# Optimization experiments

Measured on AMD Instinct MI355X. Metric: run time of the kernel, lower is better.

Reference implementation:

```python
import jax, jax.numpy as jnp
import numpy as np

SEQ, BATCH, IN, HS = 512, 64, 512, 1024
FORGET_BIAS = 0.0

def setup_inputs() -> dict:
    key = jax.random.key(0)
    ks = jax.random.split(key, 6)
    stdv = 1.0 / np.sqrt(HS)
    u = lambda k, shape: jax.random.uniform(k, shape, jnp.float32, -stdv, stdv)
    return {
        "x": jax.random.normal(ks[0], (SEQ, BATCH, IN), jnp.float32),
        "W": u(ks[1], (IN + HS, 4 * HS)),
        "bias": u(ks[2], (4 * HS,)),
        "peep_i": u(ks[3], (HS,)),
        "peep_f": u(ks[4], (HS,)),
        "peep_o": u(ks[5], (HS,)),
    }

def reference(x, W, bias, peep_i, peep_f, peep_o):
    bs = x.shape[1]
    c0 = jnp.zeros((bs, HS), x.dtype)
    h0 = jnp.zeros((bs, HS), x.dtype)

    def step(carry, x_t):
        c, h = carry
        # gates: [B, 4H] = [x_t | h] @ W + bias
        gates = jnp.concatenate([x_t, h], axis=1) @ W + bias
        i_t, j_t, f_t, o_t = jnp.split(gates, 4, axis=1)
        c_new = (jax.nn.sigmoid(f_t + FORGET_BIAS + c * peep_f) * c
                 + jax.nn.sigmoid(i_t + c * peep_i) * jnp.tanh(j_t))
        h_new = jax.nn.sigmoid(o_t + c_new * peep_o) * jnp.tanh(c_new)
        return (c_new, h_new), h_new

    (c_T, h_T), hidden_seq = jax.lax.scan(step, (c0, h0), x)
    return hidden_seq, (c_T, h_T)
```

## Files before the change

kernel.cpp:

```cpp
#include <hip/hip_runtime.h>
#include <hip/hip_bf16.h>


#define SEQN 512
#define BATCH 64
#define INDIM 512
#define HSZ 1024
#define NWG 128
#define DEPTH 64

typedef __attribute__((ext_vector_type(8))) short s16x8;
typedef __attribute__((ext_vector_type(4))) float f32x4;
typedef __attribute__((ext_vector_type(2))) float f32x2;
typedef __attribute__((ext_vector_type(4))) int i32x4;
typedef unsigned long long u64;

__device__ __forceinline__ short f2bf(float f) {
  __hip_bfloat16 b = __float2bfloat16(f);
  short s;
  __builtin_memcpy(&s, &b, 2);
  return s;
}
__device__ __forceinline__ float sigf(float x) { return 1.f / (1.f + __expf(-x)); }
__device__ __forceinline__ float tanh_fast(float x) { return 2.f / (1.f + __expf(-2.f * x)) - 1.f; }

__global__ __launch_bounds__(256) void prep_w(const float* __restrict__ W,
                                              short* __restrict__ WxP,
                                              short* __restrict__ WhP) {
  int idx = blockIdx.x * 256 + threadIdx.x;
  if (idx >= 1536 * 4096) return;
  int k = idx >> 12, col = idx & 4095;
  short b = f2bf(W[idx]);
  int gate = col >> 10, hidx = col & 1023;
  int g = hidx >> 3, off = hidx & 7;
  int pc = off * 4 + gate;
  if (k < 512) {
    WxP[(size_t)(((g * 64 + (k >> 3)) * 32 + pc) << 3) + (k & 7)] = b;
  } else {
    int kh = k - 512;
    WhP[(size_t)(((g * 128 + (kh >> 3)) * 32 + pc) << 3) + (kh & 7)] = b;
  }
}

__global__ __launch_bounds__(256) void prep_x(const float* __restrict__ x,
                                              short* __restrict__ xbp) {
  int idx = blockIdx.x * 256 + threadIdx.x;
  if (idx >= SEQN * 64 * 64) return;
  int kb = idx & 63, m = (idx >> 6) & 63, t = idx >> 12;
  const float4* xp = reinterpret_cast<const float4*>(x + ((size_t)t * 64 + m) * 512 + kb * 8);
  float4 a = xp[0], c = xp[1];
  s16x8 v;
  v[0] = f2bf(a.x); v[1] = f2bf(a.y); v[2] = f2bf(a.z); v[3] = f2bf(a.w);
  v[4] = f2bf(c.x); v[5] = f2bf(c.y); v[6] = f2bf(c.z); v[7] = f2bf(c.w);
  reinterpret_cast<s16x8*>(xbp)[((size_t)t * 64 + kb) * 64 + m] = v;
}

__global__ __launch_bounds__(256, 1) void lstm_seq(const short* __restrict__ xbp,
                                                   const short* __restrict__ WhP,
                                                   const short* __restrict__ WxP,
                                                   const float* __restrict__ bias,
                                                   const float* __restrict__ peep_i,
                                                   const float* __restrict__ peep_f,
                                                   const float* __restrict__ peep_o,
                                                   u64* hqt,
                                                   float* __restrict__ out) {
  __shared__ short WhS[32768];
  __shared__ short WxS[16384];
  __shared__ float outS[512];
  int g = blockIdx.x;
  int tid = threadIdx.x, w = tid >> 6, l = tid & 63;
  {
    const s16x8* src = reinterpret_cast<const s16x8*>(WhP + (size_t)g * 32768);
    s16x8* dst = reinterpret_cast<s16x8*>(WhS);
#pragma unroll
    for (int i = 0; i < 16; ++i) dst[i * 256 + tid] = src[i * 256 + tid];
    const s16x8* src2 = reinterpret_cast<const s16x8*>(WxP + (size_t)g * 16384);
    s16x8* dst2 = reinterpret_cast<s16x8*>(WxS);
#pragma unroll
    for (int i = 0; i < 8; ++i) dst2[i * 256 + tid] = src2[i * 256 + tid];
  }
  int m = w * 16 + (l & 15), q4 = l >> 4, l15 = l & 15;
  int c0 = g * 8 + q4, c1 = c0 + 4;
  float bi0 = bias[c0], bj0 = bias[1024 + c0], bf0 = bias[2048 + c0], bo0 = bias[3072 + c0];
  float bi1 = bias[c1], bj1 = bias[1024 + c1], bf1 = bias[2048 + c1], bo1 = bias[3072 + c1];
  float pi0 = peep_i[c0], pf0 = peep_f[c0], po0 = peep_o[c0];
  float pi1 = peep_i[c1], pf1 = peep_f[c1], po1 = peep_o[c1];
  float cr0 = 0.f, cr1 = 0.f;
  s16x8* WhS16 = reinterpret_cast<s16x8*>(WhS);
  s16x8* WxS16 = reinterpret_cast<s16x8*>(WxS);
  __syncthreads();

#define LOADG(BANK, G)                                                                   \
  {                                                                                      \
    _Pragma("unroll") for (int i = 0; i < 16; ++i) {                                     \
      int kb_ = ((G) * 8 + (i >> 1)) * 4 + q4;                                           \
      BANK[i] = *reinterpret_cast<const i32x4*>(rdq + kb_ * 256 + m * 4 + (i & 1) * 2);  \
    }                                                                                    \
  }
#define RELOADG(BANK, G)                                                                 \
  {                                                                                      \
    _Pragma("unroll") for (int i = 0; i < 16; ++i) {                                     \
      int kb_ = ((G) * 8 + (i >> 1)) * 4 + q4;                                           \
      const u64* p_ = rdq + kb_ * 256 + m * 4 + (i & 1) * 2;                             \
      asm volatile("global_load_dwordx4 %0, %1, off sc0 sc1" : "=v"(BANK[i]) : "v"(p_)); \
    }                                                                                    \
    asm volatile("s_waitcnt vmcnt(0)" ::: "memory");                                     \
    __builtin_amdgcn_sched_barrier(0);                                                   \
  }
#define CHECKG(BANK, G)                                                                  \
  {                                                                                      \
    int guard = 0;                                                                       \
    while (true) {                                                                       \
      bool ok = true;                                                                    \
      _Pragma("unroll") for (int i = 0; i < 16; ++i) ok &=                               \
          ((unsigned)BANK[i][1] == (unsigned)t) & ((unsigned)BANK[i][3] == (unsigned)t); \
      if (__all((int)ok)) break;                                                         \
      if (++guard > (1 << 13)) break;                         \
      RELOADG(BANK, G);                                                                  \
    }                                                                                    \
  }
#define MFMAG(BANK, G)                                                                   \
  {                                                                                      \
    _Pragma("unroll") for (int kk2 = 0; kk2 < 8; ++kk2) {                                \
      int kb_ = ((G) * 8 + kk2) * 4 + q4;                                                \
      unsigned d0 = (unsigned)BANK[kk2 * 2][0], d1 = (unsigned)BANK[kk2 * 2][2];         \
      unsigned d2 = (unsigned)BANK[kk2 * 2 + 1][0], d3 = (unsigned)BANK[kk2 * 2 + 1][2]; \
      union { unsigned u[4]; s16x8 v; } bu;                                              \
      bu.u[0] = (d0 & 0xFFFFu) | (d1 << 16);                                             \
      bu.u[1] = (d2 & 0xFFFFu) | (d3 << 16);                                             \
      bu.u[2] = (d0 >> 16) | (d1 & 0xFFFF0000u);                                         \
      bu.u[3] = (d2 >> 16) | (d3 & 0xFFFF0000u);                                        \
      s16x8 a0 = WhS16[kb_ * 32 + l15];                                                  \
      s16x8 a1 = WhS16[kb_ * 32 + 16 + l15];                                             \
      acc0 = __builtin_amdgcn_mfma_f32_16x16x32_bf16(a0, bu.v, acc0, 0, 0, 0);           \
      acc1 = __builtin_amdgcn_mfma_f32_16x16x32_bf16(a1, bu.v, acc1, 0, 0, 0);           \
    }                                                                                    \
  }

  for (int t = 0; t < SEQN; ++t) {
    f32x4 acc0 = {0.f, 0.f, 0.f, 0.f}, acc1 = {0.f, 0.f, 0.f, 0.f};
    {
      const s16x8* xt = reinterpret_cast<const s16x8*>(xbp) + (size_t)t * 4096;
#pragma unroll 4
      for (int kk = 0; kk < 16; ++kk) {
        int kb = kk * 4 + q4;
        s16x8 bx = xt[kb * 64 + m];
        s16x8 a0 = WxS16[kb * 32 + l15];
        s16x8 a1 = WxS16[kb * 32 + 16 + l15];
        acc0 = __builtin_amdgcn_mfma_f32_16x16x32_bf16(a0, bx, acc0, 0, 0, 0);
        acc1 = __builtin_amdgcn_mfma_f32_16x16x32_bf16(a1, bx, acc1, 0, 0, 0);
      }
    }
    if (t > 0) {
      const u64* rdq = hqt + (size_t)(t & (DEPTH - 1)) * 32768;
      i32x4 hA[16], hB[16];
      LOADG(hA, 0);
      LOADG(hB, 1);
      CHECKG(hA, 0);
      MFMAG(hA, 0);
      LOADG(hA, 2);
      CHECKG(hB, 1);
      MFMAG(hB, 1);
      LOADG(hB, 3);
      CHECKG(hA, 2);
      MFMAG(hA, 2);
      CHECKG(hB, 3);
      MFMAG(hB, 3);
    }
    float i0 = sigf(acc0[0] + bi0 + cr0 * pi0);
    float f0 = sigf(acc0[2] + bf0 + cr0 * pf0);
    float cn0 = f0 * cr0 + i0 * tanh_fast(acc0[1] + bj0);
    float o0 = sigf(acc0[3] + bo0 + cn0 * po0);
    float h0 = o0 * tanh_fast(cn0);
    cr0 = cn0;
    float i1 = sigf(acc1[0] + bi1 + cr1 * pi1);
    float f1 = sigf(acc1[2] + bf1 + cr1 * pf1);
    float cn1 = f1 * cr1 + i1 * tanh_fast(acc1[1] + bj1);
    float o1 = sigf(acc1[3] + bo1 + cn1 * po1);
    float h1 = o1 * tanh_fast(cn1);
    cr1 = cn1;
    {
      u64 q = ((u64)(unsigned)(t + 1) << 32) |
              ((u64)(unsigned short)f2bf(h1) << 16) | (u64)(unsigned short)f2bf(h0);
      (void)__hip_atomic_exchange(
          hqt + (size_t)((t + 1) & (DEPTH - 1)) * 32768 + g * 256 + m * 4 + q4, q,
          __ATOMIC_RELAXED, __HIP_MEMORY_SCOPE_AGENT);
    }
    outS[w * 128 + l15 * 8 + q4] = h0;
    outS[w * 128 + l15 * 8 + q4 + 4] = h1;
    {
      f32x2 v = *reinterpret_cast<f32x2*>(&outS[w * 128 + (l >> 2) * 8 + (l & 3) * 2]);
      int row = w * 16 + (l >> 2), col = g * 8 + (l & 3) * 2;
      __builtin_nontemporal_store(
          v, reinterpret_cast<f32x2*>(out + (size_t)t * 65536 + (size_t)row * 1024 + col));
    }
    if (t == SEQN - 1) {
      out[33554432ull + (size_t)m * 1024 + c0] = cn0;
      out[33554432ull + (size_t)m * 1024 + c1] = cn1;
      out[33619968ull + (size_t)m * 1024 + c0] = h0;
      out[33619968ull + (size_t)m * 1024 + c1] = h1;
    }
  }
#undef LOADG
#undef RELOADG
#undef CHECKG
#undef MFMAG
}

extern "C" void kernel_launch(void* const* d_in, const int* in_sizes, int n_in,
                              void* d_out, int out_size, void* d_ws, size_t ws_size,
                              hipStream_t stream) {
  const float* x      = (const float*)d_in[0];
  const float* W      = (const float*)d_in[1];
  const float* bias   = (const float*)d_in[2];
  const float* peep_i = (const float*)d_in[3];
  const float* peep_f = (const float*)d_in[4];
  const float* peep_o = (const float*)d_in[5];
  char* ws = (char*)d_ws;
  short* WxP = (short*)(ws);
  short* WhP = (short*)(ws + 4194304ull);
  short* xbp = (short*)(ws + 12582912ull);
  u64* hqt   = (u64*)(ws + 46137344ull);
  (void)hipMemsetAsync(hqt, 0, 16777216ull, stream);
  prep_w<<<24576, 256, 0, stream>>>(W, WxP, WhP);
  prep_x<<<8192, 256, 0, stream>>>(x, xbp);
  lstm_seq<<<NWG, 256, 0, stream>>>(xbp, WhP, WxP, bias, peep_i, peep_f, peep_o, hqt,
                                    (float*)d_out);
}
```

Before: 2.587 ms.

## Split LSTM hidden-state exchange into packed data buffer plus per-wave flags

Replaces the per-element tagged h exchange with two pieces. h values are packed densely in bf16, four per u64, into a separate buffer, and a small flag array holds one step tag per workgroup per wave. Readers poll only the flag line, sleeping between polls, then stream the packed h with plain overlapped loads. This halves the exchanged bytes and removes the per-element tag checks and reload loops. In exchange, writers must drain their stores before publishing the flag, and the ring depth shrinks to 4, which relies on the lock-step progress between workgroups to stay correct.

```diff
diff --git a/kernel.cpp b/kernel.cpp
--- a/kernel.cpp
+++ b/kernel.cpp
@@ -7,7 +7,7 @@
 #define INDIM 512
 #define HSZ 1024
 #define NWG 128
-#define DEPTH 64
+#define DEPTH 4
 
 typedef __attribute__((ext_vector_type(8))) short s16x8;
 typedef __attribute__((ext_vector_type(4))) float f32x4;
@@ -62,7 +62,8 @@
                                                    const float* __restrict__ peep_i,
                                                    const float* __restrict__ peep_f,
                                                    const float* __restrict__ peep_o,
-                                                   u64* hqt,
+                                                   u64* hq,
+                                                   u64* tagv,
                                                    float* __restrict__ out) {
   __shared__ short WhS[32768];
   __shared__ short WxS[16384];
@@ -90,52 +91,28 @@
   s16x8* WxS16 = reinterpret_cast<s16x8*>(WxS);
   __syncthreads();
 
-#define LOADG(BANK, G)                                                                   \
+#define ISSUE(BANK, G)                                                                   \
   {                                                                                      \
-    _Pragma("unroll") for (int i = 0; i < 16; ++i) {                                     \
-      int kb_ = ((G) * 8 + (i >> 1)) * 4 + q4;                                           \
-      BANK[i] = *reinterpret_cast<const i32x4*>(rdq + kb_ * 256 + m * 4 + (i & 1) * 2);  \
-    }                                                                                    \
-  }
-#define RELOADG(BANK, G)                                                                 \
-  {                                                                                      \
-    _Pragma("unroll") for (int i = 0; i < 16; ++i) {                                     \
-      int kb_ = ((G) * 8 + (i >> 1)) * 4 + q4;                                           \
-      const u64* p_ = rdq + kb_ * 256 + m * 4 + (i & 1) * 2;                             \
+    _Pragma("unroll") for (int i = 0; i < 8; ++i) {                                      \
+      const u64* p_ = rdq + (size_t)((((G) * 8 + i) * 4 + q4) * 128 + m * 2);            \
       asm volatile("global_load_dwordx4 %0, %1, off sc0 sc1" : "=v"(BANK[i]) : "v"(p_)); \
     }                                                                                    \
-    asm volatile("s_waitcnt vmcnt(0)" ::: "memory");                                     \
-    __builtin_amdgcn_sched_barrier(0);                                                   \
-  }
-#define CHECKG(BANK, G)                                                                  \
-  {                                                                                      \
-    int guard = 0;                                                                       \
-    while (true) {                                                                       \
-      bool ok = true;                                                                    \
-      _Pragma("unroll") for (int i = 0; i < 16; ++i) ok &=                               \
-          ((unsigned)BANK[i][1] == (unsigned)t) & ((unsigned)BANK[i][3] == (unsigned)t); \
-      if (__all((int)ok)) break;                                                         \
-      if (++guard > (1 << 13)) break;                         \
-      RELOADG(BANK, G);                                                                  \
-    }                                                                                    \
   }
 #define MFMAG(BANK, G)                                                                   \
   {                                                                                      \
-    _Pragma("unroll") for (int kk2 = 0; kk2 < 8; ++kk2) {                                \
-      int kb_ = ((G) * 8 + kk2) * 4 + q4;                                                \
-      unsigned d0 = (unsigned)BANK[kk2 * 2][0], d1 = (unsigned)BANK[kk2 * 2][2];         \
-      unsigned d2 = (unsigned)BANK[kk2 * 2 + 1][0], d3 = (unsigned)BANK[kk2 * 2 + 1][2]; \
-      union { unsigned u[4]; s16x8 v; } bu;                                              \
-      bu.u[0] = (d0 & 0xFFFFu) | (d1 << 16);                                             \
-      bu.u[1] = (d2 & 0xFFFFu) | (d3 << 16);                                             \
-      bu.u[2] = (d0 >> 16) | (d1 & 0xFFFF0000u);                                         \
-      bu.u[3] = (d2 >> 16) | (d3 & 0xFFFF0000u);                                        \
+    _Pragma("unroll") for (int i = 0; i < 8; ++i) {                                      \
+      int kb_ = ((G) * 8 + i) * 4 + q4;                                                  \
+      s16x8 bv;                                                                          \
+      __builtin_memcpy(&bv, &BANK[i], 16);                                               \
       s16x8 a0 = WhS16[kb_ * 32 + l15];                                                  \
       s16x8 a1 = WhS16[kb_ * 32 + 16 + l15];                                             \
-      acc0 = __builtin_amdgcn_mfma_f32_16x16x32_bf16(a0, bu.v, acc0, 0, 0, 0);           \
-      acc1 = __builtin_amdgcn_mfma_f32_16x16x32_bf16(a1, bu.v, acc1, 0, 0, 0);           \
+      acc0 = __builtin_amdgcn_mfma_f32_16x16x32_bf16(a0, bv, acc0, 0, 0, 0);             \
+      acc1 = __builtin_amdgcn_mfma_f32_16x16x32_bf16(a1, bv, acc1, 0, 0, 0);             \
     }                                                                                    \
   }
+#define VWAIT(N)                                                                         \
+  asm volatile("s_waitcnt vmcnt(" #N ")" ::: "memory");                                  \
+  __builtin_amdgcn_sched_barrier(0);
 
   for (int t = 0; t < SEQN; ++t) {
     f32x4 acc0 = {0.f, 0.f, 0.f, 0.f}, acc1 = {0.f, 0.f, 0.f, 0.f};
@@ -152,19 +129,32 @@
       }
     }
     if (t > 0) {
-      const u64* rdq = hqt + (size_t)(t & (DEPTH - 1)) * 32768;
-      i32x4 hA[16], hB[16];
-      LOADG(hA, 0);
-      LOADG(hB, 1);
-      CHECKG(hA, 0);
+      {
+        const u64* gp = tagv + (size_t)(t & (DEPTH - 1)) * 512 + (size_t)w * 128 + 2 * l;
+        int guard = 0;
+        while (true) {
+          i32x4 gv;
+          asm volatile("global_load_dwordx4 %0, %1, off sc0 sc1" : "=v"(gv) : "v"(gp));
+          asm volatile("s_waitcnt vmcnt(0)" ::: "memory");
+          __builtin_amdgcn_sched_barrier(0);
+          if (__all((int)((gv[0] == t) & (gv[2] == t)))) break;
+          if (++guard > (1 << 13)) break;
+          __builtin_amdgcn_s_sleep(1);
+        }
+      }
+      const u64* rdq = hq + (size_t)(t & (DEPTH - 1)) * 16384;
+      i32x4 hA[8], hB[8];
+      ISSUE(hA, 0);
+      ISSUE(hB, 1);
+      VWAIT(8);
       MFMAG(hA, 0);
-      LOADG(hA, 2);
-      CHECKG(hB, 1);
+      ISSUE(hA, 2);
+      VWAIT(8);
       MFMAG(hB, 1);
-      LOADG(hB, 3);
-      CHECKG(hA, 2);
+      ISSUE(hB, 3);
+      VWAIT(8);
       MFMAG(hA, 2);
-      CHECKG(hB, 3);
+      VWAIT(0);
       MFMAG(hB, 3);
     }
     float i0 = sigf(acc0[0] + bi0 + cr0 * pi0);
@@ -180,12 +170,31 @@
     float h1 = o1 * tanh_fast(cn1);
     cr1 = cn1;
     {
-      u64 q = ((u64)(unsigned)(t + 1) << 32) |
-              ((u64)(unsigned short)f2bf(h1) << 16) | (u64)(unsigned short)f2bf(h0);
+      unsigned myh = (unsigned)(unsigned short)f2bf(h0) |
+                     ((unsigned)(unsigned short)f2bf(h1) << 16);
+      int base = l15;
+      unsigned va = (unsigned)__shfl((int)myh, base);
+      unsigned vb = (unsigned)__shfl((int)myh, base + 16);
+      unsigned vc = (unsigned)__shfl((int)myh, base + 32);
+      unsigned vd = (unsigned)__shfl((int)myh, base + 48);
+      if (q4 < 2) {
+        u64 q;
+        if (q4 == 0)
+          q = (u64)(va & 0xFFFFu) | ((u64)(vb & 0xFFFFu) << 16) |
+              ((u64)(vc & 0xFFFFu) << 32) | ((u64)(vd & 0xFFFFu) << 48);
+        else
+          q = (u64)(va >> 16) | ((u64)(vb >> 16) << 16) |
+              ((u64)(vc >> 16) << 32) | ((u64)(vd >> 16) << 48);
+        (void)__hip_atomic_exchange(
+            hq + (size_t)((t + 1) & (DEPTH - 1)) * 16384 + g * 128 + m * 2 + q4, q,
+            __ATOMIC_RELAXED, __HIP_MEMORY_SCOPE_AGENT);
+      }
+    }
+    asm volatile("s_waitcnt vmcnt(0)" ::: "memory");
+    if (l == 0)
       (void)__hip_atomic_exchange(
-          hqt + (size_t)((t + 1) & (DEPTH - 1)) * 32768 + g * 256 + m * 4 + q4, q,
-          __ATOMIC_RELAXED, __HIP_MEMORY_SCOPE_AGENT);
-    }
+          tagv + (size_t)((t + 1) & (DEPTH - 1)) * 512 + (size_t)w * 128 + g,
+          (u64)(unsigned)(t + 1), __ATOMIC_RELAXED, __HIP_MEMORY_SCOPE_AGENT);
     outS[w * 128 + l15 * 8 + q4] = h0;
     outS[w * 128 + l15 * 8 + q4 + 4] = h1;
     {
@@ -201,10 +210,9 @@
       out[33619968ull + (size_t)m * 1024 + c1] = h1;
     }
   }
-#undef LOADG
-#undef RELOADG
-#undef CHECKG
+#undef ISSUE
 #undef MFMAG
+#undef VWAIT
 }
 
 extern "C" void kernel_launch(void* const* d_in, const int* in_sizes, int n_in,
@@ -220,10 +228,11 @@
   short* WxP = (short*)(ws);
   short* WhP = (short*)(ws + 4194304ull);
   short* xbp = (short*)(ws + 12582912ull);
-  u64* hqt   = (u64*)(ws + 46137344ull);
-  (void)hipMemsetAsync(hqt, 0, 16777216ull, stream);
+  u64* hq    = (u64*)(ws + 46137344ull);
+  u64* tagv  = (u64*)(ws + 46661632ull);
+  (void)hipMemsetAsync(tagv, 0, 16384ull, stream);
   prep_w<<<24576, 256, 0, stream>>>(W, WxP, WhP);
   prep_x<<<8192, 256, 0, stream>>>(x, xbp);
-  lstm_seq<<<NWG, 256, 0, stream>>>(xbp, WhP, WxP, bias, peep_i, peep_f, peep_o, hqt,
-                                    (float*)d_out);
-}
+  lstm_seq<<<NWG, 256, 0, stream>>>(xbp, WhP, WxP, bias, peep_i, peep_f, peep_o, hq,
+                                    tagv, (float*)d_out);
+}
```

Result: faster. 2.140 ms (-17.3%).
